# Optimization experiments

Hardware: AMD Instinct MI355X
Metric: run time of the kernel (lower is better)

The kernel has to match this reference:

```python
import jax, jax.numpy as jnp
import numpy as np

ACT_BITS = 8
QMAX = float(2 ** ACT_BITS - 1)  # unsigned fake-quant range [0, 255]


def setup_inputs() -> dict:
    key = jax.random.key(0)
    k_x, k_w, k_b = jax.random.split(key, 3)
    B, S, D_IN, D_OUT = 4, 2048, 4096, 4096
    x = jax.random.normal(k_x, (B, S, D_IN), dtype=jnp.float32)
    # per-tensor int-quantized weight [out_features, in_features]
    qweight = jax.random.randint(k_w, (D_OUT, D_IN), 0, 256, dtype=jnp.int32)
    scale = jnp.asarray(0.01, dtype=jnp.float32)
    zero_point = jnp.asarray(128, dtype=jnp.int32)
    bias = jax.random.normal(k_b, (D_OUT,), dtype=jnp.float32) * 0.02
    act_scale = jnp.asarray(0.02, dtype=jnp.float32)
    act_zero_point = jnp.asarray(128, dtype=jnp.int32)
    return {
        "x": x,
        "qweight": qweight,
        "scale": scale,
        "zero_point": zero_point,
        "bias": bias,
        "act_scale": act_scale,
        "act_zero_point": act_zero_point,
    }


def reference(x, qweight, scale, zero_point, bias, act_scale, act_zero_point):
    # --- activation fake-quant (quantize then dequantize, per-tensor) ---
    azp = act_zero_point.astype(jnp.float32)
    x_q = jnp.clip(jnp.round(x / act_scale) + azp, 0.0, QMAX)
    x_fq = (x_q - azp) * act_scale
    # --- weight dequant: (q - zp) * scale, per-tensor scalar params ---
    w = (qweight.astype(jnp.float32) - zero_point.astype(jnp.float32)) * scale
    # --- dense GEMM: F.linear(x, w, bias) = x @ w.T + bias ---
    return jnp.einsum("bsd,od->bso", x_fq, w) + bias
```

## Files before the change

kernel.cpp:

```cpp
#include <hip/hip_runtime.h>
#include <hip/hip_bf16.h>


typedef __attribute__((ext_vector_type(4))) int int4v;

#define BM 256
#define BN 128
#define BK 128

__global__ __launch_bounds__(256) void quant_x_kernel(
    const float4* __restrict__ x, unsigned int* __restrict__ xq,
    const float* __restrict__ act_scale_p, const int* __restrict__ act_zp_p,
    int n4)
{
    int g = blockIdx.x * blockDim.x + threadIdx.x;
    if (g >= n4) return;
    const float s   = act_scale_p[0];
    const float azp = (float)act_zp_p[0];
    const float lo = -azp, hi = 255.0f - azp;
    float4 v = x[g];
    float f0 = fminf(fmaxf(rintf(v.x / s), lo), hi);
    float f1 = fminf(fmaxf(rintf(v.y / s), lo), hi);
    float f2 = fminf(fmaxf(rintf(v.z / s), lo), hi);
    float f3 = fminf(fmaxf(rintf(v.w / s), lo), hi);
    unsigned int b0 = (unsigned int)(int)f0 & 0xff;
    unsigned int b1 = (unsigned int)(int)f1 & 0xff;
    unsigned int b2 = (unsigned int)(int)f2 & 0xff;
    unsigned int b3 = (unsigned int)(int)f3 & 0xff;
    xq[g] = b0 | (b1 << 8) | (b2 << 16) | (b3 << 24);
}

__global__ __launch_bounds__(256) void quant_w_kernel(
    const int4* __restrict__ qw, unsigned int* __restrict__ wq,
    const int* __restrict__ zp_p, int n4)
{
    int g = blockIdx.x * blockDim.x + threadIdx.x;
    if (g >= n4) return;
    const int zp = zp_p[0];
    int4 v = qw[g];
    unsigned int b0 = (unsigned int)(v.x - zp) & 0xff;
    unsigned int b1 = (unsigned int)(v.y - zp) & 0xff;
    unsigned int b2 = (unsigned int)(v.z - zp) & 0xff;
    unsigned int b3 = (unsigned int)(v.w - zp) & 0xff;
    wq[g] = b0 | (b1 << 8) | (b2 << 16) | (b3 << 24);
}

#define ASYNC_CP16(gp, lp)                                                      \
    __builtin_amdgcn_global_load_lds(                                           \
        (const __attribute__((address_space(1))) unsigned int*)(gp),            \
        (__attribute__((address_space(3))) unsigned int*)(lp), 16, 0, 0)

__global__ __launch_bounds__(256, 2) void gemm_i8_kernel(
    const signed char* __restrict__ A,
    const signed char* __restrict__ B,
    const float* __restrict__ bias,
    const float* __restrict__ scale_p, const float* __restrict__ act_scale_p,
    float* __restrict__ C, int M, int N, int K)
{
    __shared__ __align__(16) signed char As[BM * BK];
    __shared__ __align__(16) signed char Bs[BN * BK];

    const int tid  = threadIdx.x;
    const int lane = tid & 63;
    const int wave = tid >> 6;
    const int bm = blockIdx.y * BM;
    const int bn = blockIdx.x * BN;

    const int srow = tid >> 3;
    const int scol = ((tid & 7) ^ (srow & 7)) * 16;
    const signed char* aP = A + (size_t)(bm + srow) * K + scol;
    const signed char* bP = B + (size_t)(bn + srow) * K + scol;
    signed char* asD = &As[(size_t)tid * 16];
    signed char* bsD = &Bs[(size_t)tid * 16];

    const int wm = wave * 64;
    const int fr = lane & 15;
    const int g4 = lane >> 4;
    const int x7 = fr & 7;

    int4v acc[4][8] = {};

    for (int k0 = 0; k0 < K; k0 += BK) {
#pragma unroll
        for (int r = 0; r < 8; r++)
            ASYNC_CP16(aP + (size_t)r * 32 * K, asD + r * 4096);
#pragma unroll
        for (int r = 0; r < 4; r++)
            ASYNC_CP16(bP + (size_t)r * 32 * K, bsD + r * 4096);
        aP += BK; bP += BK;
        __syncthreads();

#pragma unroll
        for (int kk = 0; kk < 2; kk++) {
            const int ko = ((kk * 4 + g4) ^ x7) * 16;
            int4v af[4], bf[8];
#pragma unroll
            for (int i = 0; i < 4; i++)
                af[i] = *(const int4v*)&As[(wm + i * 16 + fr) * BK + ko];
#pragma unroll
            for (int j = 0; j < 8; j++)
                bf[j] = *(const int4v*)&Bs[(j * 16 + fr) * BK + ko];
#pragma unroll
            for (int i = 0; i < 4; i++)
#pragma unroll
                for (int j = 0; j < 8; j++)
                    acc[i][j] = __builtin_amdgcn_mfma_i32_16x16x64_i8(
                        af[i], bf[j], acc[i][j], 0, 0, 0);
        }
        __syncthreads();
    }

    const float sc = scale_p[0] * act_scale_p[0];
    const int crow = (lane >> 4) * 4;
    const int ccol = lane & 15;
#pragma unroll
    for (int i = 0; i < 4; i++) {
        const int m = bm + wm + i * 16 + crow;
#pragma unroll
        for (int j = 0; j < 8; j++) {
            const int n = bn + j * 16 + ccol;
            const float bv = bias[n];
#pragma unroll
            for (int r = 0; r < 4; r++) {
                C[(size_t)(m + r) * N + n] = (float)acc[i][j][r] * sc + bv;
            }
        }
    }
}

extern "C" void kernel_launch(void* const* d_in, const int* in_sizes, int n_in,
                              void* d_out, int out_size, void* d_ws, size_t ws_size,
                              hipStream_t stream) {
    const float* x         = (const float*)d_in[0];
    const int*   qw        = (const int*)  d_in[1];
    const float* scale     = (const float*)d_in[2];
    const int*   zp        = (const int*)  d_in[3];
    const float* bias      = (const float*)d_in[4];
    const float* act_scale = (const float*)d_in[5];
    const int*   act_zp    = (const int*)  d_in[6];
    float* out = (float*)d_out;

    const int D_OUT = in_sizes[4];
    const int D_IN  = in_sizes[1] / D_OUT;
    const int M = in_sizes[0] / D_IN;
    const int N = D_OUT, K = D_IN;

    signed char* xq = (signed char*)d_ws;
    signed char* wq = xq + (size_t)M * K;

    const int n4x = (M * K) / 4;
    quant_x_kernel<<<(n4x + 255) / 256, 256, 0, stream>>>(
        (const float4*)x, (unsigned int*)xq, act_scale, act_zp, n4x);

    const int n4w = (N * K) / 4;
    quant_w_kernel<<<(n4w + 255) / 256, 256, 0, stream>>>(
        (const int4*)qw, (unsigned int*)wq, zp, n4w);

    dim3 grid(N / BN, M / BM);
    gemm_i8_kernel<<<grid, 256, 0, stream>>>(xq, wq, bias, scale, act_scale,
                                             out, M, N, K);
}
```

Baseline: 384.9 us.

## Use 256x256 tiles, 8 waves, double-buffered LDS with interleaved async loads

Raises the GEMM block tile from 256x128 to 256x256 with 512 threads arranged as a 2x4 wave grid. LDS is double-buffered and each K step is split into four quadrant sub-phases. Async global-to-LDS copies for the next tiles are interleaved between the MFMA phases, with explicit vmcnt waits, barriers and setprio. The goal is to hide global-load latency behind compute and raise arithmetic intensity per byte loaded. In exchange it uses 128KB of LDS per block (likely one block per CU), adds many barriers, and carries fragile hand-tuned wait counts.

```diff
diff --git a/kernel.cpp b/kernel.cpp
--- a/kernel.cpp
+++ b/kernel.cpp
@@ -1,11 +1,10 @@
 #include <hip/hip_runtime.h>
-#include <hip/hip_bf16.h>
 
 
 typedef __attribute__((ext_vector_type(4))) int int4v;
 
 #define BM 256
-#define BN 128
+#define BN 256
 #define BK 128
 
 __global__ __launch_bounds__(256) void quant_x_kernel(
@@ -50,19 +49,21 @@
         (const __attribute__((address_space(1))) unsigned int*)(gp),            \
         (__attribute__((address_space(3))) unsigned int*)(lp), 16, 0, 0)
 
-__global__ __launch_bounds__(256, 2) void gemm_i8_kernel(
+__global__ __launch_bounds__(512, 2) void gemm_i8_kernel(
     const signed char* __restrict__ A,
     const signed char* __restrict__ B,
     const float* __restrict__ bias,
     const float* __restrict__ scale_p, const float* __restrict__ act_scale_p,
     float* __restrict__ C, int M, int N, int K)
 {
-    __shared__ __align__(16) signed char As[BM * BK];
-    __shared__ __align__(16) signed char Bs[BN * BK];
+    __shared__ __align__(16) signed char As[2][BM * BK];
+    __shared__ __align__(16) signed char Bs[2][BN * BK];
 
     const int tid  = threadIdx.x;
     const int lane = tid & 63;
     const int wave = tid >> 6;
+    const int wm = wave >> 2;
+    const int wn = wave & 3;
     const int bm = blockIdx.y * BM;
     const int bn = blockIdx.x * BN;
 
@@ -70,58 +71,121 @@
     const int scol = ((tid & 7) ^ (srow & 7)) * 16;
     const signed char* aP = A + (size_t)(bm + srow) * K + scol;
     const signed char* bP = B + (size_t)(bn + srow) * K + scol;
-    signed char* asD = &As[(size_t)tid * 16];
-    signed char* bsD = &Bs[(size_t)tid * 16];
-
-    const int wm = wave * 64;
+
     const int fr = lane & 15;
     const int g4 = lane >> 4;
     const int x7 = fr & 7;
-
-    int4v acc[4][8] = {};
-
-    for (int k0 = 0; k0 < K; k0 += BK) {
-#pragma unroll
-        for (int r = 0; r < 8; r++)
-            ASYNC_CP16(aP + (size_t)r * 32 * K, asD + r * 4096);
-#pragma unroll
-        for (int r = 0; r < 4; r++)
-            ASYNC_CP16(bP + (size_t)r * 32 * K, bsD + r * 4096);
-        aP += BK; bP += BK;
-        __syncthreads();
-
-#pragma unroll
-        for (int kk = 0; kk < 2; kk++) {
-            const int ko = ((kk * 4 + g4) ^ x7) * 16;
-            int4v af[4], bf[8];
-#pragma unroll
-            for (int i = 0; i < 4; i++)
-                af[i] = *(const int4v*)&As[(wm + i * 16 + fr) * BK + ko];
-#pragma unroll
-            for (int j = 0; j < 8; j++)
-                bf[j] = *(const int4v*)&Bs[(j * 16 + fr) * BK + ko];
-#pragma unroll
-            for (int i = 0; i < 4; i++)
-#pragma unroll
-                for (int j = 0; j < 8; j++)
-                    acc[i][j] = __builtin_amdgcn_mfma_i32_16x16x64_i8(
-                        af[i], bf[j], acc[i][j], 0, 0, 0);
+    const int ko0 = ((0 * 4 + g4) ^ x7) * 16;
+    const int ko1 = ((1 * 4 + g4) ^ x7) * 16;
+
+    const int aRd = (wm * 64 + fr) * BK;
+    const int bRd = (wn * 32 + fr) * BK;
+
+    int4v acc[8][4] = {};
+    const int NT = K / BK;
+
+#define SR(gp, L, H, R, T)                                                     \
+    ASYNC_CP16((gp) + (size_t)((H) * 128 + (R) * 64) * K + (size_t)(T) * BK,   \
+               (L) + (H) * 16384 + (R) * 8192 + tid * 16)
+#define SU(gp, L, H, T) do { SR(gp, L, H, 0, T); SR(gp, L, H, 1, T); } while (0)
+
+    SU(aP, As[0], 0, 0);
+    SU(bP, Bs[0], 0, 0);
+    SU(bP, Bs[0], 1, 0);
+    SU(aP, As[0], 1, 0);
+    if (NT > 1) {
+        SU(aP, As[1], 0, 1);
+        SU(bP, Bs[1], 0, 1);
+        asm volatile("s_waitcnt vmcnt(6)");
+    } else {
+        asm volatile("s_waitcnt vmcnt(2)");
+    }
+    __builtin_amdgcn_s_barrier();
+
+#define LDA(RH)                                                                \
+    _Pragma("unroll") for (int i2 = 0; i2 < 4; ++i2) {                         \
+        af[i2][0] = *(const int4v*)&cA[aRd + (RH) * 16384 + i2 * 2048 + ko0];  \
+        af[i2][1] = *(const int4v*)&cA[aRd + (RH) * 16384 + i2 * 2048 + ko1];  \
+    }
+#define LDB(CH)                                                                \
+    _Pragma("unroll") for (int j2 = 0; j2 < 2; ++j2) {                         \
+        bf[j2][0] = *(const int4v*)&cB[bRd + (CH) * 16384 + j2 * 2048 + ko0];  \
+        bf[j2][1] = *(const int4v*)&cB[bRd + (CH) * 16384 + j2 * 2048 + ko1];  \
+    }
+#define MMA(RH, CH)                                                            \
+    _Pragma("unroll") for (int ks = 0; ks < 2; ++ks)                           \
+    _Pragma("unroll") for (int i2 = 0; i2 < 4; ++i2)                           \
+    _Pragma("unroll") for (int j2 = 0; j2 < 2; ++j2)                           \
+        acc[(RH) * 4 + i2][(CH) * 2 + j2] =                                    \
+            __builtin_amdgcn_mfma_i32_16x16x64_i8(                             \
+                af[i2][ks], bf[j2][ks], acc[(RH) * 4 + i2][(CH) * 2 + j2],     \
+                0, 0, 0);
+
+#pragma unroll 2
+    for (int t = 0; t < NT; ++t) {
+        signed char* cA = As[t & 1];
+        signed char* cB = Bs[t & 1];
+        signed char* nA = As[(t & 1) ^ 1];
+        signed char* nB = Bs[(t & 1) ^ 1];
+        const bool p1 = (t + 1 < NT);
+        const bool p2 = (t + 2 < NT);
+        int4v af[4][2], bf[2][2];
+
+        LDA(0); LDB(0);
+        if (p1) SU(bP, nB, 1, t + 1);
+        __builtin_amdgcn_s_barrier();
+        asm volatile("s_waitcnt lgkmcnt(0)");
+        __builtin_amdgcn_s_setprio(1);
+        MMA(0, 0);
+        __builtin_amdgcn_s_setprio(0);
+        __builtin_amdgcn_s_barrier();
+
+        LDB(1);
+        if (p1) SU(aP, nA, 1, t + 1);
+        __builtin_amdgcn_s_barrier();
+        asm volatile("s_waitcnt lgkmcnt(0)");
+        __builtin_amdgcn_s_setprio(1);
+        MMA(0, 1);
+        __builtin_amdgcn_s_setprio(0);
+        if (p1) asm volatile("s_waitcnt vmcnt(8)");
+        else    asm volatile("s_waitcnt vmcnt(0)");
+        __builtin_amdgcn_s_barrier();
+
+        LDA(1); LDB(0);
+        if (p2) SU(aP, cA, 0, t + 2);
+        __builtin_amdgcn_s_barrier();
+        asm volatile("s_waitcnt lgkmcnt(0)");
+        __builtin_amdgcn_s_setprio(1);
+        MMA(1, 0);
+        __builtin_amdgcn_s_setprio(0);
+        __builtin_amdgcn_s_barrier();
+
+        LDB(1);
+        if (p2) SU(bP, cB, 0, t + 2);
+        __builtin_amdgcn_s_barrier();
+        asm volatile("s_waitcnt lgkmcnt(0)");
+        __builtin_amdgcn_s_setprio(1);
+        MMA(1, 1);
+        __builtin_amdgcn_s_setprio(0);
+        if (p1) {
+            if (p2) asm volatile("s_waitcnt vmcnt(6)");
+            else    asm volatile("s_waitcnt vmcnt(2)");
         }
-        __syncthreads();
+        __builtin_amdgcn_s_barrier();
     }
 
     const float sc = scale_p[0] * act_scale_p[0];
     const int crow = (lane >> 4) * 4;
     const int ccol = lane & 15;
 #pragma unroll
-    for (int i = 0; i < 4; i++) {
-        const int m = bm + wm + i * 16 + crow;
+    for (int i = 0; i < 8; ++i) {
+        const int m = bm + (i >> 2) * 128 + wm * 64 + (i & 3) * 16 + crow;
 #pragma unroll
-        for (int j = 0; j < 8; j++) {
-            const int n = bn + j * 16 + ccol;
+        for (int j = 0; j < 4; ++j) {
+            const int n = bn + (j >> 1) * 128 + wn * 32 + (j & 1) * 16 + ccol;
             const float bv = bias[n];
 #pragma unroll
-            for (int r = 0; r < 4; r++) {
+            for (int r = 0; r < 4; ++r) {
                 C[(size_t)(m + r) * N + n] = (float)acc[i][j][r] * sc + bv;
             }
         }
@@ -157,6 +221,6 @@
         (const int4*)qw, (unsigned int*)wq, zp, n4w);
 
     dim3 grid(N / BN, M / BM);
-    gemm_i8_kernel<<<grid, 256, 0, stream>>>(xq, wq, bias, scale, act_scale,
+    gemm_i8_kernel<<<grid, 512, 0, stream>>>(xq, wq, bias, scale, act_scale,
                                              out, M, N, K);
 }
```

Result: slower. 397.2 us (+3.2%).
